# Kernel optimization log

Measured on AMD Instinct MI355X. Metric: run time of the kernel, lower is better.

The kernel has to match this reference:

```python
import jax, jax.numpy as jnp
import numpy as np

B, S, T = 128, 512, 256


def setup_inputs() -> dict:
    key = jax.random.key(0)
    k1, k2, k3, k4 = jax.random.split(key, 4)
    emissions = jax.random.normal(k1, (B, S, T), dtype=jnp.float32)
    mask = jnp.ones((B, S), dtype=bool)
    transitions = jax.random.normal(k2, (T, T), dtype=jnp.float32)
    start_transitions = jax.random.normal(k3, (T,), dtype=jnp.float32)
    end_transitions = jax.random.normal(k4, (T,), dtype=jnp.float32)
    return {
        "emissions": emissions,
        "mask": mask,
        "transitions": transitions,
        "start_transitions": start_transitions,
        "end_transitions": end_transitions,
    }


def reference(emissions, mask, transitions, start_transitions, end_transitions):
    """Batched Viterbi decode. Returns (paths [B,S] int32, best_scores [B] f32).

    Faithful to CRFLayer._viterbi_decode: score_0 = start + em_0; at each step
    next[i,j] = score[i] + trans[i,j] + em_t[j], take max/argmax over i; add
    end_transitions at the end; backtrack via backpointers. Masked (padded)
    steps carry score through unchanged with identity backpointers, so padded
    tail positions replicate the last valid tag (mask is all-ones here, so
    output equals the original's full-length paths).
    """
    Bn, Sn, Tn = emissions.shape
    ident = jnp.arange(Tn, dtype=jnp.int32)
    score0 = start_transitions[None, :] + emissions[:, 0]  # [B,T]

    em_ts = jnp.swapaxes(emissions, 0, 1)[1:]  # [S-1,B,T]
    m_ts = jnp.swapaxes(mask, 0, 1)[1:]        # [S-1,B]

    def step(score, inp):
        em_t, m_t = inp
        # nxt[b,i,j] = score[b,i] + trans[i,j] + em_t[b,j]
        nxt = score[:, :, None] + transitions[None, :, :] + em_t[:, None, :]
        best = jnp.max(nxt, axis=1)                    # [B,T]
        idx = jnp.argmax(nxt, axis=1).astype(jnp.int32)  # [B,T] best prev tag
        m = m_t[:, None]
        new_score = jnp.where(m, best, score)
        bp = jnp.where(m, idx, ident[None, :])
        return new_score, bp

    final_score, history = jax.lax.scan(step, score0, (em_ts, m_ts))  # history [S-1,B,T]
    final_score = final_score + end_transitions[None, :]
    best_scores = jnp.max(final_score, axis=1)                         # [B]
    last_tag = jnp.argmax(final_score, axis=1).astype(jnp.int32)       # [B]

    def back(tag, hist_t):
        prev = jnp.take_along_axis(hist_t, tag[:, None], axis=1)[:, 0]
        return prev, tag  # carry prev tag, emit current tag

    first_tag, tags_rest = jax.lax.scan(back, last_tag, history, reverse=True)
    # tags_rest[t] = tag at position t+1; first_tag = tag at position 0
    paths = jnp.concatenate([first_tag[:, None], jnp.swapaxes(tags_rest, 0, 1)], axis=1)
    return paths, best_scores
```

## Files before the change

kernel.cpp:

```cpp
#include <hip/hip_runtime.h>

#define Bn 128
#define Sn 512
#define Tn 256
#define LPAD 320

template <int CTRL>
__device__ __forceinline__ float dpp_fmax(float v) {
  int x = __builtin_amdgcn_mov_dpp(__float_as_int(v), CTRL, 0xF, 0xF, true);
  return fmaxf(v, __int_as_float(x));
}
__device__ __forceinline__ float row_fmax16(float v) {
  v = dpp_fmax<0x128>(v);
  v = dpp_fmax<0x124>(v);
  v = dpp_fmax<0x122>(v);
  v = dpp_fmax<0x121>(v);
  return v;
}
__device__ __forceinline__ float wave_fmax64(float v) {
  v = row_fmax16(v);
  int x = __builtin_amdgcn_ds_swizzle(__float_as_int(v), 0x401F);
  v = fmaxf(v, __int_as_float(x));
  v = fmaxf(v, __shfl_xor(v, 32));
  return v;
}

__global__ __launch_bounds__(256) void transpose_kernel(
    const float* __restrict__ tr, float* __restrict__ trT) {
  int idx = blockIdx.x * 256 + threadIdx.x;
  int i = idx >> 8;
  int j = idx & 255;
  trT[j * Tn + i] = tr[i * Tn + j];
}

__global__ __launch_bounds__(1024, 4) void viterbi_fwd(
    const float* __restrict__ em,
    const float* __restrict__ trans,
    const float* __restrict__ start,
    float* __restrict__ scores)
{
  const int b    = blockIdx.x;
  const int tid  = threadIdx.x;
  const int lane = tid & 63;
  const int w    = tid >> 6;
  const int cg   = lane >> 4;
  const int ip   = lane & 15;
  const int jbase = w * 16 + cg * 4;
  const int i0    = ip * 16;
  const bool writer = (ip == 0);
  const int idxW = jbase + ((jbase >> 4) << 2);
  const int idxR = 20 * ip;

  __shared__ float sbuf[2][LPAD];

  float4 tr[16];
#pragma unroll
  for (int k = 0; k < 16; ++k)
    tr[k] = *reinterpret_cast<const float4*>(trans + (i0 + k) * Tn + jbase);

  const float* emb = em + (size_t)b * Sn * Tn;
  float* scb = scores + (size_t)b * Sn * Tn;

  if (tid < 64) {
    int j4 = tid * 4;
    float4 st = *reinterpret_cast<const float4*>(start + j4);
    float4 e0 = *reinterpret_cast<const float4*>(emb + j4);
    float4 s0 = make_float4(st.x + e0.x, st.y + e0.y, st.z + e0.z, st.w + e0.w);
    *reinterpret_cast<float4*>(&sbuf[0][j4 + ((tid >> 2) << 2)]) = s0;
    *reinterpret_cast<float4*>(scb + j4) = s0;
  }

  const float* emPre = emb + 2 * Tn + jbase;
  float* scW = scb + Tn + jbase;
  float4 eC;
  if (writer) eC = *reinterpret_cast<const float4*>(emb + Tn + jbase);
  float4 pA;
  float* pW = nullptr;
  __syncthreads();

  int cur = 0;
  for (int t = 1; t < Sn; ++t) {
    const float* sp = &sbuf[cur][idxR];
    float4 a0 = *reinterpret_cast<const float4*>(sp);
    float4 a1 = *reinterpret_cast<const float4*>(sp + 4);
    float4 a2 = *reinterpret_cast<const float4*>(sp + 8);
    float4 a3 = *reinterpret_cast<const float4*>(sp + 12);

    float4 eN;
    if (writer) {
      if (t > 1) *reinterpret_cast<float4*>(pW) = pA;
      const float* p = (t + 1 < Sn) ? emPre : emPre - Tn;
      eN = *reinterpret_cast<const float4*>(p);
    }

    float se[16] = {a0.x,a0.y,a0.z,a0.w, a1.x,a1.y,a1.z,a1.w,
                    a2.x,a2.y,a2.z,a2.w, a3.x,a3.y,a3.z,a3.w};

    float m0 = se[0] + tr[0].x;
    float m1 = se[0] + tr[0].y;
    float m2 = se[0] + tr[0].z;
    float m3 = se[0] + tr[0].w;
#pragma unroll
    for (int k = 1; k < 15; k += 2) {
      m0 = fmaxf(fmaxf(m0, se[k]+tr[k].x), se[k+1]+tr[k+1].x);
      m1 = fmaxf(fmaxf(m1, se[k]+tr[k].y), se[k+1]+tr[k+1].y);
      m2 = fmaxf(fmaxf(m2, se[k]+tr[k].z), se[k+1]+tr[k+1].z);
      m3 = fmaxf(fmaxf(m3, se[k]+tr[k].w), se[k+1]+tr[k+1].w);
    }
    m0 = fmaxf(m0, se[15]+tr[15].x);
    m1 = fmaxf(m1, se[15]+tr[15].y);
    m2 = fmaxf(m2, se[15]+tr[15].z);
    m3 = fmaxf(m3, se[15]+tr[15].w);

    m0 = row_fmax16(m0);
    m1 = row_fmax16(m1);
    m2 = row_fmax16(m2);
    m3 = row_fmax16(m3);

    if (writer) {
      float4 ns = make_float4(m0 + eC.x, m1 + eC.y, m2 + eC.z, m3 + eC.w);
      *reinterpret_cast<float4*>(&sbuf[cur ^ 1][idxW]) = ns;
      pA = ns; pW = scW;
      eC = eN;
    }
    emPre += Tn;
    scW   += Tn;
    cur ^= 1;
    __syncthreads();
  }
  if (writer) *reinterpret_cast<float4*>(pW) = pA;
}

__global__ __launch_bounds__(64) void viterbi_bwd(
    const float* __restrict__ em,
    const float* __restrict__ trT,
    const float* __restrict__ endt,
    const float* __restrict__ scores,
    float* __restrict__ out)
{
  const int b = blockIdx.x;
  const int lane = threadIdx.x;
  const float* scb = scores + (size_t)b * Sn * Tn;
  const float* emb = em + (size_t)b * Sn * Tn;
  const int base = lane * 4;
  const int BIG = 1 << 30;

  float4 s = *reinterpret_cast<const float4*>(scb + (size_t)(Sn - 1) * Tn + base);
  float4 e = *reinterpret_cast<const float4*>(endt + base);
  float d0 = s.x + e.x, d1 = s.y + e.y, d2 = s.z + e.z, d3 = s.w + e.w;
  float bv = fmaxf(fmaxf(fmaxf(d0, d1), d2), d3);
  bv = wave_fmax64(bv);
  int li = BIG;
  if (d3 == bv) li = base + 3;
  if (d2 == bv) li = base + 2;
  if (d1 == bv) li = base + 1;
  if (d0 == bv) li = base;
  unsigned long long mk = __ballot(li != BIG);
  int fl = (int)__ffsll(mk) - 1;
  int tag = __shfl(li, fl);
  if (lane == 0) {
    out[Bn * Sn + b] = bv;
    out[b * Sn + (Sn - 1)] = (float)tag;
  }

  float4 sv  = *reinterpret_cast<const float4*>(scb + (size_t)(Sn - 2) * Tn + base);
  float4 sv2 = *reinterpret_cast<const float4*>(scb + (size_t)(Sn - 3) * Tn + base);
  float4 e4  = *reinterpret_cast<const float4*>(emb + (size_t)(Sn - 1) * Tn + base);
  float4 e42 = *reinterpret_cast<const float4*>(emb + (size_t)(Sn - 2) * Tn + base);

  for (int k = Sn - 2; k >= 0; --k) {
    float4 tv = *reinterpret_cast<const float4*>(trT + (size_t)tag * Tn + base);
    int kp = (k >= 2) ? k - 2 : 0;
    int ke = (k >= 1) ? k - 1 : 0;
    float4 sv_nn = *reinterpret_cast<const float4*>(scb + (size_t)kp * Tn + base);
    float4 e4_nn = *reinterpret_cast<const float4*>(emb + (size_t)ke * Tn + base);

    int comp = tag & 3, src = tag >> 2;
    float es = (comp == 0) ? e4.x : (comp == 1) ? e4.y
             : (comp == 2) ? e4.z : e4.w;
    float ev = __shfl(es, src);

    d0 = (sv.x + tv.x) + ev;
    d1 = (sv.y + tv.y) + ev;
    d2 = (sv.z + tv.z) + ev;
    d3 = (sv.w + tv.w) + ev;
    bv = fmaxf(fmaxf(fmaxf(d0, d1), d2), d3);
    bv = wave_fmax64(bv);
    li = BIG;
    if (d3 == bv) li = base + 3;
    if (d2 == bv) li = base + 2;
    if (d1 == bv) li = base + 1;
    if (d0 == bv) li = base;
    mk = __ballot(li != BIG);
    fl = (int)__ffsll(mk) - 1;
    tag = __shfl(li, fl);
    if (lane == 0) out[b * Sn + k] = (float)tag;
    sv = sv2; sv2 = sv_nn;
    e4 = e42; e42 = e4_nn;
  }
}

extern "C" void kernel_launch(void* const* d_in, const int* in_sizes, int n_in,
                              void* d_out, int out_size, void* d_ws, size_t ws_size,
                              hipStream_t stream) {
  const float* em    = (const float*)d_in[0];
  const float* trans = (const float*)d_in[2];
  const float* start = (const float*)d_in[3];
  const float* endt  = (const float*)d_in[4];
  float* out = (float*)d_out;

  float* scores = (float*)d_ws;
  float* trT = (float*)((char*)d_ws + (size_t)Bn * Sn * Tn * 4);

  transpose_kernel<<<Tn * Tn / 256, 256, 0, stream>>>(trans, trT);
  viterbi_fwd<<<Bn, 1024, 0, stream>>>(em, trans, start, scores);
  viterbi_bwd<<<Bn, 64, 0, stream>>>(em, trT, endt, scores, out);
}
```

Measured before the change: 763.2 us.

## Shrink forward Viterbi block to 256 threads with packed transitions and buffer backtrack tags

The forward kernel drops from 1024 to 256 threads per batch. Each lane now keeps a 16x16 transition tile in registers as packed float2 pairs, broadcasts scores within quads using DPP, and reduces across lanes with DPP, swizzle and shuffle, so every lane writes output. This aims to cut barrier cost and idle writer lanes on the sequential recurrence, in exchange for much higher register pressure. The backward kernel also warms the transposed transitions into cache, uses nontemporal loads for the score and emission streams, and buffers tags in shared memory before one coalesced write at the end.

```diff
diff --git a/kernel.cpp b/kernel.cpp
--- a/kernel.cpp
+++ b/kernel.cpp
@@ -3,12 +3,18 @@
 #define Bn 128
 #define Sn 512
 #define Tn 256
-#define LPAD 320
-
+
+typedef float v2f __attribute__((ext_vector_type(2)));
+typedef float v4f __attribute__((ext_vector_type(4)));
+
+template <int CTRL>
+__device__ __forceinline__ float dpp_movf(float v) {
+  return __int_as_float(
+      __builtin_amdgcn_mov_dpp(__float_as_int(v), CTRL, 0xF, 0xF, true));
+}
 template <int CTRL>
 __device__ __forceinline__ float dpp_fmax(float v) {
-  int x = __builtin_amdgcn_mov_dpp(__float_as_int(v), CTRL, 0xF, 0xF, true);
-  return fmaxf(v, __int_as_float(x));
+  return fmaxf(v, dpp_movf<CTRL>(v));
 }
 __device__ __forceinline__ float row_fmax16(float v) {
   v = dpp_fmax<0x128>(v);
@@ -24,6 +30,10 @@
   v = fmaxf(v, __shfl_xor(v, 32));
   return v;
 }
+__device__ __forceinline__ float swz_xor16(float v) {
+  return __int_as_float(
+      __builtin_amdgcn_ds_swizzle(__float_as_int(v), 0x401F));
+}
 
 __global__ __launch_bounds__(256) void transpose_kernel(
     const float* __restrict__ tr, float* __restrict__ trT) {
@@ -33,7 +43,7 @@
   trT[j * Tn + i] = tr[i * Tn + j];
 }
 
-__global__ __launch_bounds__(1024, 4) void viterbi_fwd(
+__global__ __launch_bounds__(256, 1) void viterbi_fwd(
     const float* __restrict__ em,
     const float* __restrict__ trans,
     const float* __restrict__ start,
@@ -43,20 +53,32 @@
   const int tid  = threadIdx.x;
   const int lane = tid & 63;
   const int w    = tid >> 6;
-  const int cg   = lane >> 4;
-  const int ip   = lane & 15;
-  const int jbase = w * 16 + cg * 4;
-  const int i0    = ip * 16;
-  const bool writer = (ip == 0);
-  const int idxW = jbase + ((jbase >> 4) << 2);
-  const int idxR = 20 * ip;
-
-  __shared__ float sbuf[2][LPAD];
-
-  float4 tr[16];
-#pragma unroll
-  for (int k = 0; k < 16; ++k)
-    tr[k] = *reinterpret_cast<const float4*>(trans + (i0 + k) * Tn + jbase);
+  const int q    = lane >> 2;
+  const int r    = lane & 3;
+  const int b4   = (lane >> 4) & 1;
+  const int b5   = (lane >> 5) & 1;
+  const int jpre = w * 64 + r * 16;
+  const int jfin = jpre + 8 * b4 + 4 * b5;
+  const int i0   = q * 16;
+
+  __shared__ float sbuf[2][Tn];
+
+  v2f tpk[16][8];
+#pragma unroll
+  for (int k = 0; k < 16; ++k) {
+    const float* rw = trans + (i0 + k) * Tn + jpre;
+    float4 x0 = *reinterpret_cast<const float4*>(rw);
+    float4 x1 = *reinterpret_cast<const float4*>(rw + 4);
+    float4 x2 = *reinterpret_cast<const float4*>(rw + 8);
+    float4 x3 = *reinterpret_cast<const float4*>(rw + 12);
+    float e16[16] = {x0.x,x0.y,x0.z,x0.w, x1.x,x1.y,x1.z,x1.w,
+                     x2.x,x2.y,x2.z,x2.w, x3.x,x3.y,x3.z,x3.w};
+#pragma unroll
+    for (int c = 0; c < 16; ++c) {
+      if (k & 1) tpk[c][k >> 1].y = e16[c];
+      else       tpk[c][k >> 1].x = e16[c];
+    }
+  }
 
   const float* emb = em + (size_t)b * Sn * Tn;
   float* scb = scores + (size_t)b * Sn * Tn;
@@ -66,72 +88,106 @@
     float4 st = *reinterpret_cast<const float4*>(start + j4);
     float4 e0 = *reinterpret_cast<const float4*>(emb + j4);
     float4 s0 = make_float4(st.x + e0.x, st.y + e0.y, st.z + e0.z, st.w + e0.w);
-    *reinterpret_cast<float4*>(&sbuf[0][j4 + ((tid >> 2) << 2)]) = s0;
+    *reinterpret_cast<float4*>(&sbuf[0][j4]) = s0;
     *reinterpret_cast<float4*>(scb + j4) = s0;
   }
 
-  const float* emPre = emb + 2 * Tn + jbase;
-  float* scW = scb + Tn + jbase;
-  float4 eC;
-  if (writer) eC = *reinterpret_cast<const float4*>(emb + Tn + jbase);
+  const float* emPre = emb + 2 * Tn + jfin;
+  float* scW = scb + Tn + jfin;
+  float4 eC = *reinterpret_cast<const float4*>(emb + Tn + jfin);
   float4 pA;
   float* pW = nullptr;
   __syncthreads();
 
   int cur = 0;
   for (int t = 1; t < Sn; ++t) {
-    const float* sp = &sbuf[cur][idxR];
-    float4 a0 = *reinterpret_cast<const float4*>(sp);
-    float4 a1 = *reinterpret_cast<const float4*>(sp + 4);
-    float4 a2 = *reinterpret_cast<const float4*>(sp + 8);
-    float4 a3 = *reinterpret_cast<const float4*>(sp + 12);
-
-    float4 eN;
-    if (writer) {
-      if (t > 1) *reinterpret_cast<float4*>(pW) = pA;
-      const float* p = (t + 1 < Sn) ? emPre : emPre - Tn;
-      eN = *reinterpret_cast<const float4*>(p);
-    }
-
-    float se[16] = {a0.x,a0.y,a0.z,a0.w, a1.x,a1.y,a1.z,a1.w,
-                    a2.x,a2.y,a2.z,a2.w, a3.x,a3.y,a3.z,a3.w};
-
-    float m0 = se[0] + tr[0].x;
-    float m1 = se[0] + tr[0].y;
-    float m2 = se[0] + tr[0].z;
-    float m3 = se[0] + tr[0].w;
-#pragma unroll
-    for (int k = 1; k < 15; k += 2) {
-      m0 = fmaxf(fmaxf(m0, se[k]+tr[k].x), se[k+1]+tr[k+1].x);
-      m1 = fmaxf(fmaxf(m1, se[k]+tr[k].y), se[k+1]+tr[k+1].y);
-      m2 = fmaxf(fmaxf(m2, se[k]+tr[k].z), se[k+1]+tr[k+1].z);
-      m3 = fmaxf(fmaxf(m3, se[k]+tr[k].w), se[k+1]+tr[k+1].w);
-    }
-    m0 = fmaxf(m0, se[15]+tr[15].x);
-    m1 = fmaxf(m1, se[15]+tr[15].y);
-    m2 = fmaxf(m2, se[15]+tr[15].z);
-    m3 = fmaxf(m3, se[15]+tr[15].w);
-
-    m0 = row_fmax16(m0);
-    m1 = row_fmax16(m1);
-    m2 = row_fmax16(m2);
-    m3 = row_fmax16(m3);
-
-    if (writer) {
-      float4 ns = make_float4(m0 + eC.x, m1 + eC.y, m2 + eC.z, m3 + eC.w);
-      *reinterpret_cast<float4*>(&sbuf[cur ^ 1][idxW]) = ns;
-      pA = ns; pW = scW;
-      eC = eN;
-    }
+    float4 se = *reinterpret_cast<const float4*>(&sbuf[cur][4 * lane]);
+
+    if (t > 1) *reinterpret_cast<float4*>(pW) = pA;
+    const float* p = (t + 1 < Sn) ? emPre : emPre - Tn;
+    float4 eN = *reinterpret_cast<const float4*>(p);
+
+    v2f sp[8];
+    {
+      float4 bc;
+      bc.x = dpp_movf<0x00>(se.x); bc.y = dpp_movf<0x00>(se.y);
+      bc.z = dpp_movf<0x00>(se.z); bc.w = dpp_movf<0x00>(se.w);
+      sp[0] = (v2f){bc.x, bc.y}; sp[1] = (v2f){bc.z, bc.w};
+      bc.x = dpp_movf<0x55>(se.x); bc.y = dpp_movf<0x55>(se.y);
+      bc.z = dpp_movf<0x55>(se.z); bc.w = dpp_movf<0x55>(se.w);
+      sp[2] = (v2f){bc.x, bc.y}; sp[3] = (v2f){bc.z, bc.w};
+      bc.x = dpp_movf<0xAA>(se.x); bc.y = dpp_movf<0xAA>(se.y);
+      bc.z = dpp_movf<0xAA>(se.z); bc.w = dpp_movf<0xAA>(se.w);
+      sp[4] = (v2f){bc.x, bc.y}; sp[5] = (v2f){bc.z, bc.w};
+      bc.x = dpp_movf<0xFF>(se.x); bc.y = dpp_movf<0xFF>(se.y);
+      bc.z = dpp_movf<0xFF>(se.z); bc.w = dpp_movf<0xFF>(se.w);
+      sp[6] = (v2f){bc.x, bc.y}; sp[7] = (v2f){bc.z, bc.w};
+    }
+
+    float m[16];
+#pragma unroll
+    for (int c = 0; c < 16; ++c) {
+      v2f a0 = sp[0] + tpk[c][0];
+      v2f a1 = sp[1] + tpk[c][1];
+      v2f a2 = sp[2] + tpk[c][2];
+      v2f a3 = sp[3] + tpk[c][3];
+      v2f a4 = sp[4] + tpk[c][4];
+      v2f a5 = sp[5] + tpk[c][5];
+      v2f a6 = sp[6] + tpk[c][6];
+      v2f a7 = sp[7] + tpk[c][7];
+      float mm = fmaxf(fmaxf(a0.x, a0.y), a1.x);
+      mm = fmaxf(fmaxf(mm, a1.y), a2.x);
+      mm = fmaxf(fmaxf(mm, a2.y), a3.x);
+      mm = fmaxf(fmaxf(mm, a3.y), a4.x);
+      mm = fmaxf(fmaxf(mm, a4.y), a5.x);
+      mm = fmaxf(fmaxf(mm, a5.y), a6.x);
+      mm = fmaxf(fmaxf(mm, a6.y), a7.x);
+      m[c] = fmaxf(mm, a7.y);
+    }
+
+#pragma unroll
+    for (int c = 0; c < 16; ++c) {
+      m[c] = dpp_fmax<0x124>(m[c]);
+      m[c] = dpp_fmax<0x128>(m[c]);
+    }
+
+    float kp[8];
+#pragma unroll
+    for (int cc = 0; cc < 8; ++cc) {
+      float snd = b4 ? m[cc] : m[cc + 8];
+      float kep = b4 ? m[cc + 8] : m[cc];
+      kp[cc] = fmaxf(kep, swz_xor16(snd));
+    }
+    float f0, f1, f2, f3;
+    {
+      float s0 = b5 ? kp[0] : kp[4];
+      float k0 = b5 ? kp[4] : kp[0];
+      f0 = fmaxf(k0, __shfl_xor(s0, 32));
+      float s1 = b5 ? kp[1] : kp[5];
+      float k1 = b5 ? kp[5] : kp[1];
+      f1 = fmaxf(k1, __shfl_xor(s1, 32));
+      float s2 = b5 ? kp[2] : kp[6];
+      float k2 = b5 ? kp[6] : kp[2];
+      f2 = fmaxf(k2, __shfl_xor(s2, 32));
+      float s3 = b5 ? kp[3] : kp[7];
+      float k3 = b5 ? kp[7] : kp[3];
+      f3 = fmaxf(k3, __shfl_xor(s3, 32));
+    }
+
+    float4 ns = make_float4(f0 + eC.x, f1 + eC.y, f2 + eC.z, f3 + eC.w);
+    *reinterpret_cast<float4*>(&sbuf[cur ^ 1][jfin]) = ns;
+    pA = ns; pW = scW;
+    eC = eN;
+
     emPre += Tn;
     scW   += Tn;
     cur ^= 1;
     __syncthreads();
   }
-  if (writer) *reinterpret_cast<float4*>(pW) = pA;
-}
-
-__global__ __launch_bounds__(64) void viterbi_bwd(
+  *reinterpret_cast<float4*>(pW) = pA;
+}
+
+__global__ __launch_bounds__(64, 1) void viterbi_bwd(
     const float* __restrict__ em,
     const float* __restrict__ trT,
     const float* __restrict__ endt,
@@ -145,9 +201,21 @@
   const int base = lane * 4;
   const int BIG = 1 << 30;
 
+  __shared__ unsigned char pbuf[Sn];
+
+  float warm = 0.0f;
+  for (int off = base; off < Tn * Tn; off += 256) {
+    float4 wv = *reinterpret_cast<const float4*>(trT + off);
+    warm += wv.x + wv.y + wv.z + wv.w;
+  }
+  warm *= 0.0f;
+
   float4 s = *reinterpret_cast<const float4*>(scb + (size_t)(Sn - 1) * Tn + base);
   float4 e = *reinterpret_cast<const float4*>(endt + base);
-  float d0 = s.x + e.x, d1 = s.y + e.y, d2 = s.z + e.z, d3 = s.w + e.w;
+  float d0 = (s.x + e.x) + warm;
+  float d1 = (s.y + e.y) + warm;
+  float d2 = (s.z + e.z) + warm;
+  float d3 = (s.w + e.w) + warm;
   float bv = fmaxf(fmaxf(fmaxf(d0, d1), d2), d3);
   bv = wave_fmax64(bv);
   int li = BIG;
@@ -160,20 +228,26 @@
   int tag = __shfl(li, fl);
   if (lane == 0) {
     out[Bn * Sn + b] = bv;
-    out[b * Sn + (Sn - 1)] = (float)tag;
-  }
-
-  float4 sv  = *reinterpret_cast<const float4*>(scb + (size_t)(Sn - 2) * Tn + base);
-  float4 sv2 = *reinterpret_cast<const float4*>(scb + (size_t)(Sn - 3) * Tn + base);
-  float4 e4  = *reinterpret_cast<const float4*>(emb + (size_t)(Sn - 1) * Tn + base);
-  float4 e42 = *reinterpret_cast<const float4*>(emb + (size_t)(Sn - 2) * Tn + base);
+    pbuf[Sn - 1] = (unsigned char)tag;
+  }
+
+  v4f sv  = __builtin_nontemporal_load(
+      reinterpret_cast<const v4f*>(scb + (size_t)(Sn - 2) * Tn + base));
+  v4f sv2 = __builtin_nontemporal_load(
+      reinterpret_cast<const v4f*>(scb + (size_t)(Sn - 3) * Tn + base));
+  v4f e4  = __builtin_nontemporal_load(
+      reinterpret_cast<const v4f*>(emb + (size_t)(Sn - 1) * Tn + base));
+  v4f e42 = __builtin_nontemporal_load(
+      reinterpret_cast<const v4f*>(emb + (size_t)(Sn - 2) * Tn + base));
 
   for (int k = Sn - 2; k >= 0; --k) {
     float4 tv = *reinterpret_cast<const float4*>(trT + (size_t)tag * Tn + base);
     int kp = (k >= 2) ? k - 2 : 0;
     int ke = (k >= 1) ? k - 1 : 0;
-    float4 sv_nn = *reinterpret_cast<const float4*>(scb + (size_t)kp * Tn + base);
-    float4 e4_nn = *reinterpret_cast<const float4*>(emb + (size_t)ke * Tn + base);
+    v4f sv_nn = __builtin_nontemporal_load(
+        reinterpret_cast<const v4f*>(scb + (size_t)kp * Tn + base));
+    v4f e4_nn = __builtin_nontemporal_load(
+        reinterpret_cast<const v4f*>(emb + (size_t)ke * Tn + base));
 
     int comp = tag & 3, src = tag >> 2;
     float es = (comp == 0) ? e4.x : (comp == 1) ? e4.y
@@ -194,10 +268,14 @@
     mk = __ballot(li != BIG);
     fl = (int)__ffsll(mk) - 1;
     tag = __shfl(li, fl);
-    if (lane == 0) out[b * Sn + k] = (float)tag;
+    if (lane == 0) pbuf[k] = (unsigned char)tag;
     sv = sv2; sv2 = sv_nn;
     e4 = e42; e42 = e4_nn;
   }
+
+  __syncthreads();
+  for (int s2 = lane; s2 < Sn; s2 += 64)
+    out[(size_t)b * Sn + s2] = (float)pbuf[s2];
 }
 
 extern "C" void kernel_launch(void* const* d_in, const int* in_sizes, int n_in,
@@ -213,6 +291,6 @@
   float* trT = (float*)((char*)d_ws + (size_t)Bn * Sn * Tn * 4);
 
   transpose_kernel<<<Tn * Tn / 256, 256, 0, stream>>>(trans, trT);
-  viterbi_fwd<<<Bn, 1024, 0, stream>>>(em, trans, start, scores);
+  viterbi_fwd<<<Bn, 256, 0, stream>>>(em, trans, start, scores);
   viterbi_bwd<<<Bn, 64, 0, stream>>>(em, trT, endt, scores, out);
 }
```

Measured after the change: 990.1 us. 29.7% more time.
